# Optimization experiments

Hardware: AMD Instinct MI355X
Metric: run time of the kernel (lower is better)

## Reference

```python
import jax, jax.numpy as jnp
import numpy as np
import math

D_MODEL = 1024
NUM_HEADS = 16
HEAD_DIM = D_MODEL // NUM_HEADS
B, T = 2, 2048


def _linear_params(key, d_in, d_out):
    kw, kb = jax.random.split(key)
    s = 1.0 / math.sqrt(d_in)
    W = jax.random.uniform(kw, (d_in, d_out), jnp.float32, -s, s)
    b = jax.random.uniform(kb, (d_out,), jnp.float32, -s, s)
    return W, b


def setup_inputs() -> dict:
    key = jax.random.key(0)
    ks = jax.random.split(key, 10)
    x_real = jax.random.normal(ks[0], (B, T, D_MODEL), jnp.float32)
    x_imag = jax.random.normal(ks[1], (B, T, D_MODEL), jnp.float32)
    Wqr, bqr = _linear_params(ks[2], D_MODEL, D_MODEL)
    Wqi, bqi = _linear_params(ks[3], D_MODEL, D_MODEL)
    Wkr, bkr = _linear_params(ks[4], D_MODEL, D_MODEL)
    Wki, bki = _linear_params(ks[5], D_MODEL, D_MODEL)
    Wvr, bvr = _linear_params(ks[6], D_MODEL, D_MODEL)
    Wvi, bvi = _linear_params(ks[7], D_MODEL, D_MODEL)
    Wor, bor = _linear_params(ks[8], D_MODEL, D_MODEL)
    Woi, boi = _linear_params(ks[9], D_MODEL, D_MODEL)
    return dict(x_real=x_real, x_imag=x_imag,
                Wqr=Wqr, bqr=bqr, Wqi=Wqi, bqi=bqi,
                Wkr=Wkr, bkr=bkr, Wki=Wki, bki=bki,
                Wvr=Wvr, bvr=bvr, Wvi=Wvi, bvi=bvi,
                Wor=Wor, bor=bor, Woi=Woi, boi=boi)


def _heads(x):
    # (B,T,C) -> (B,H,T,Dh)
    b, t, _ = x.shape
    return x.reshape(b, t, NUM_HEADS, HEAD_DIM).transpose(0, 2, 1, 3)


def reference(x_real, x_imag,
              Wqr, bqr, Wqi, bqi, Wkr, bkr, Wki, bki,
              Wvr, bvr, Wvi, bvi, Wor, bor, Woi, boi):
    b, t, c = x_real.shape
    # NOTE: first two qr/qi assignments in the torch forward are dead code;
    # effective math is below.
    qr = _heads(x_real @ Wqr + bqr)
    qi = _heads(x_imag @ Wqi + bqi)
    kr = _heads(x_real @ Wkr + bkr)
    ki = _heads(x_imag @ Wki + bki)
    vr = _heads(x_real @ Wvr + bvr)
    vi = _heads(x_imag @ Wvi + bvi)
    # Re(Q K^H) score: Qr*Kr + Qi*Ki, scaled
    score = (jnp.einsum('bhtd,bhsd->bhts', qr, kr)
             + jnp.einsum('bhtd,bhsd->bhts', qi, ki)) / math.sqrt(HEAD_DIM)
    causal = jnp.triu(jnp.ones((t, t), dtype=bool), k=1)  # True above diagonal
    score = jnp.where(causal[None, None], -jnp.inf, score)
    attn = jax.nn.softmax(score, axis=-1)
    out_r = jnp.einsum('bhts,bhsd->bhtd', attn, vr).transpose(0, 2, 1, 3).reshape(b, t, c)
    out_i = jnp.einsum('bhts,bhsd->bhtd', attn, vi).transpose(0, 2, 1, 3).reshape(b, t, c)
    final_r = out_r @ Wor + bor
    final_i = out_i @ Woi + boi
    return (final_r, final_i)
```

## Files before the change

kernel.cpp:

```cpp
#include <hip/hip_runtime.h>
#include <hip/hip_bf16.h>


typedef __attribute__((ext_vector_type(8))) __bf16 bf16x8;
typedef __attribute__((ext_vector_type(4))) float f32x4;
typedef unsigned short u16;

#define L2E 1.44269504088896340736f

__device__ __forceinline__ void gl2lds16(const void* g, void* l) {
  __builtin_amdgcn_global_load_lds(
      (const __attribute__((address_space(1))) unsigned int*)g,
      (__attribute__((address_space(3))) unsigned int*)l, 16, 0, 0);
}

__device__ __forceinline__ u16 f2bf(float f) {
  union { float f; unsigned u; } v;
  v.f = f;
  unsigned r = v.u + 0x7FFFu + ((v.u >> 16) & 1u);
  return (u16)(r >> 16);
}

__global__ void cvt_bf16_2(const float* __restrict__ a, const float* __restrict__ bsrc,
                           u16* __restrict__ oa, u16* __restrict__ ob, int n) {
  const float* in = blockIdx.y ? bsrc : a;
  u16* out = blockIdx.y ? ob : oa;
  int stride = gridDim.x * blockDim.x * 4;
  for (int i = (blockIdx.x * blockDim.x + threadIdx.x) * 4; i < n; i += stride) {
    float4 v = *(const float4*)(in + i);
    ushort4 o;
    o.x = f2bf(v.x); o.y = f2bf(v.y); o.z = f2bf(v.z); o.w = f2bf(v.w);
    *(ushort4*)(out + i) = o;
  }
}

struct WPtrs { const float* w[8]; };

__global__ void cvt_w_t(WPtrs ptrs, u16* __restrict__ out) {
  __shared__ float tile[32][33];
  const float* W = ptrs.w[blockIdx.z];
  u16* o = out + ((size_t)blockIdx.z << 20);
  int tx = threadIdx.x & 31, ty = threadIdx.x >> 5;
  int bx = blockIdx.x * 32, by = blockIdx.y * 32;
#pragma unroll
  for (int k = 0; k < 4; k++) {
    int r = by + ty + k * 8;
    tile[ty + k * 8][tx] = W[(size_t)r * 1024 + bx + tx];
  }
  __syncthreads();
#pragma unroll
  for (int k = 0; k < 4; k++) {
    int n = bx + ty + k * 8;
    o[(size_t)n * 1024 + by + tx] = f2bf(tile[tx][ty + k * 8]);
  }
}

struct GemmArgs {
  const u16* A[6];
  const u16* Wt[6];
  const float* bias[6];
  void* dst[6];
  int off[6];
  float scale[6];
};

template <int MODE>
__global__ __launch_bounds__(256, 2) void gemm_bf16(GemmArgs args) {
  extern __shared__ u16 dynpad[];
  const int z = blockIdx.z;
  const u16* __restrict__ A = args.A[z];
  const u16* __restrict__ Bt = args.Wt[z];
  const float* __restrict__ bias = args.bias[z];
  const int brow = blockIdx.x * 128;
  const int bcol = blockIdx.y * 128;

  __shared__ u16 lA[2][128 * 32];
  __shared__ u16 lB[2][128 * 32];

  const int tid = threadIdx.x;
  const int w = tid >> 6, lane = tid & 63;
  const int wrow = (w >> 1) * 64, wcol = (w & 1) * 64;

  if (args.off[z] == -12345) ((volatile u16*)dynpad)[0] = 0;

  f32x4 acc[4][4] = {};

  auto stage = [&](int buf, int t) {
    int k0 = t * 32;
#pragma unroll
    for (int s = 0; s < 2; s++) {
      int q = w * 2 + s;
      int lr = q * 16 + (lane >> 2);
      int csrc = (lane & 3) ^ ((lr >> 1) & 3);
      gl2lds16(A + (size_t)(brow + lr) * 1024 + k0 + csrc * 8, &lA[buf][q * 512]);
    }
#pragma unroll
    for (int s = 0; s < 2; s++) {
      int q = w * 2 + s;
      int lr = q * 16 + (lane >> 2);
      int csrc = (lane & 3) ^ ((lr >> 1) & 3);
      gl2lds16(Bt + (size_t)(bcol + lr) * 1024 + k0 + csrc * 8, &lB[buf][q * 512]);
    }
  };

  stage(0, 0);
  __syncthreads();

  int buf = 0;
  for (int t = 0; t < 32; t++) {
    if (t + 1 < 32) stage(buf ^ 1, t + 1);
    bf16x8 a[4], b[4];
#pragma unroll
    for (int i = 0; i < 4; i++) {
      int row = wrow + i * 16 + (lane & 15);
      int cs = (lane >> 4) ^ ((row >> 1) & 3);
      a[i] = *(const bf16x8*)&lA[buf][row * 32 + cs * 8];
      int col = wcol + i * 16 + (lane & 15);
      int cs2 = (lane >> 4) ^ ((col >> 1) & 3);
      b[i] = *(const bf16x8*)&lB[buf][col * 32 + cs2 * 8];
    }
#pragma unroll
    for (int i = 0; i < 4; i++)
#pragma unroll
      for (int j = 0; j < 4; j++)
        acc[i][j] = __builtin_amdgcn_mfma_f32_16x16x32_bf16(a[i], b[j], acc[i][j], 0, 0, 0);
    __syncthreads();
    buf ^= 1;
  }

  const int off = args.off[z];
  const float scl = args.scale[z];
#pragma unroll
  for (int i = 0; i < 4; i++)
#pragma unroll
    for (int j = 0; j < 4; j++)
#pragma unroll
      for (int r = 0; r < 4; r++) {
        int grow = brow + wrow + i * 16 + (lane >> 4) * 4 + r;
        int gcol = bcol + wcol + j * 16 + (lane & 15);
        float v = (acc[i][j][r] + bias[gcol]) * scl;
        if (MODE == 0) {
          ((float*)args.dst[z])[(size_t)grow * 1024 + gcol] = v;
        } else {
          int bb = grow >> 11, tt = grow & 2047;
          int h = gcol >> 6, dh = gcol & 63;
          ((u16*)args.dst[z])[(((size_t)(bb * 16 + h) * 2048 + tt) << 7) + off + dh] = f2bf(v);
        }
      }
}

__global__ void transpose_v(const u16* __restrict__ Vc, u16* __restrict__ Vt) {
  __shared__ u16 tile[64 * 64];
  const int bh = blockIdx.z, t0 = blockIdx.x * 64, d0 = blockIdx.y * 64;
  const int tid = threadIdx.x;
  const int tl = tid >> 3, c = tid & 7;
#pragma unroll
  for (int hh = 0; hh < 2; hh++) {
    int t = tl + hh * 32;
    int sc = c ^ (t & 7) ^ ((t >> 3) & 7);
    *(bf16x8*)&tile[t * 64 + sc * 8] =
        *(const bf16x8*)&Vc[((size_t)bh * 2048 + t0 + t) * 128 + d0 + c * 8];
  }
  __syncthreads();
#pragma unroll
  for (int hh = 0; hh < 2; hh++) {
    int d = tl + hh * 32;
    bf16x8 v;
#pragma unroll
    for (int j = 0; j < 8; j++) {
      int t = c * 8 + j;
      int sc = (d >> 3) ^ (t & 7) ^ ((t >> 3) & 7);
      v[j] = ((const __bf16*)tile)[t * 64 + sc * 8 + (d & 7)];
    }
    *(bf16x8*)&Vt[((size_t)bh * 128 + d0 + d) * 2048 + t0 + c * 8] = v;
  }
}

__global__ __launch_bounds__(256, 2) void attn_kernel(
    const u16* __restrict__ Q, const u16* __restrict__ K, const u16* __restrict__ Vt,
    u16* __restrict__ Or, u16* __restrict__ Oi) {
  const int bh = blockIdx.x;
  const int ii = (int)gridDim.y - 1 - (int)blockIdx.y;
  const int tid = threadIdx.x, w = tid >> 6, lane = tid & 63;
  const int ql = lane & 15, hi = lane >> 4;
  const int b = bh >> 4, h = bh & 15;

  __shared__ u16 lK[2][64 * 128];
  __shared__ u16 lV[2][128 * 64];
  __shared__ u16 lP[4][16 * 64];

  const int qrow0 = ii * 64 + w * 16;
  const int q = qrow0 + ql;

  bf16x8 qf[4];
#pragma unroll
  for (int kk = 0; kk < 4; kk++)
    qf[kk] = *(const bf16x8*)(Q + ((size_t)bh * 2048 + q) * 128 + kk * 32 + hi * 8);

  f32x4 o[8] = {};
  float l = 0.f;

  const int ntiles = ii + 1;

  auto stageKV = [&](int buf, int jt) {
#pragma unroll
    for (int s = 0; s < 4; s++) {
      int seg = w * 4 + s;
      int srow = seg * 4 + (lane >> 4);
      int csrc = (lane & 15) ^ (srow & 15);
      gl2lds16(K + ((size_t)bh * 2048 + jt * 64 + srow) * 128 + csrc * 8, &lK[buf][seg * 512]);
    }
#pragma unroll
    for (int s = 0; s < 4; s++) {
      int seg = w * 4 + s;
      int dv = seg * 8 + (lane >> 3);
      int csrc = (lane & 7) ^ (dv & 7);
      gl2lds16(Vt + ((size_t)bh * 128 + dv) * 2048 + jt * 64 + csrc * 8, &lV[buf][seg * 512]);
    }
  };

  stageKV(0, 0);
  __syncthreads();

  int buf = 0;
  for (int jt = 0; jt < ntiles; jt++) {
    if (jt + 1 < ntiles) stageKV(buf ^ 1, jt + 1);

    f32x4 s[4] = {};
    __builtin_amdgcn_s_setprio(1);
#pragma unroll
    for (int kk = 0; kk < 4; kk++) {
#pragma unroll
      for (int j = 0; j < 4; j++) {
        int sl = j * 16 + ql;
        int cs = (kk * 4 + hi) ^ (sl & 15);
        bf16x8 kf = *(const bf16x8*)&lK[buf][sl * 128 + cs * 8];
        s[j] = __builtin_amdgcn_mfma_f32_16x16x32_bf16(kf, qf[kk], s[j], 0, 0, 0);
      }
    }
    __builtin_amdgcn_s_setprio(0);

    if (jt == ii) {
#pragma unroll
      for (int j = 0; j < 4; j++)
#pragma unroll
        for (int r = 0; r < 4; r++) {
          int kg = jt * 64 + j * 16 + hi * 4 + r;
          if (kg > q) s[j][r] = -__builtin_inff();
        }
    }

    uint2 pk[4];
#pragma unroll
    for (int j = 0; j < 4; j++) {
      float p0 = exp2f(__builtin_fmaf(s[j][0], L2E, -16.f * L2E));
      float p1 = exp2f(__builtin_fmaf(s[j][1], L2E, -16.f * L2E));
      float p2 = exp2f(__builtin_fmaf(s[j][2], L2E, -16.f * L2E));
      float p3 = exp2f(__builtin_fmaf(s[j][3], L2E, -16.f * L2E));
      l += (p0 + p1) + (p2 + p3);
      union { __bf16 hh[4]; uint2 u; } cv;
      cv.hh[0] = (__bf16)p0; cv.hh[1] = (__bf16)p1;
      cv.hh[2] = (__bf16)p2; cv.hh[3] = (__bf16)p3;
      pk[j] = cv.u;
    }

#pragma unroll
    for (int j = 0; j < 4; j++) {
      int byte_off = ql * 128 + ((j * 32 + hi * 8) ^ ((ql & 7) << 4));
      *(uint2*)((char*)&lP[w][0] + byte_off) = pk[j];
    }
    asm volatile("s_waitcnt lgkmcnt(0)" ::: "memory");
    __builtin_amdgcn_sched_barrier(0);

    __builtin_amdgcn_s_setprio(1);
#pragma unroll
    for (int kks = 0; kks < 2; kks++) {
      int pb = ql * 128 + ((kks * 64 + hi * 16) ^ ((ql & 7) << 4));
      bf16x8 pf = *(const bf16x8*)((char*)&lP[w][0] + pb);
#pragma unroll
      for (int jv = 0; jv < 8; jv++) {
        int dv = jv * 16 + ql;
        int cs = (kks * 4 + hi) ^ (dv & 7);
        bf16x8 vf = *(const bf16x8*)&lV[buf][dv * 64 + cs * 8];
        o[jv] = __builtin_amdgcn_mfma_f32_16x16x32_bf16(vf, pf, o[jv], 0, 0, 0);
      }
    }
    __builtin_amdgcn_s_setprio(0);

    __syncthreads();
    buf ^= 1;
  }

  l += __shfl_xor(l, 16);
  l += __shfl_xor(l, 32);
  float linv = 1.f / l;
  const size_t obase = ((size_t)b * 2048 + q) * 1024 + h * 64;
#pragma unroll
  for (int jv = 0; jv < 8; jv++) {
    ushort4 st;
    union { __bf16 hh[4]; ushort4 u; } cv;
    cv.hh[0] = (__bf16)(o[jv][0] * linv);
    cv.hh[1] = (__bf16)(o[jv][1] * linv);
    cv.hh[2] = (__bf16)(o[jv][2] * linv);
    cv.hh[3] = (__bf16)(o[jv][3] * linv);
    st = cv.u;
    u16* dst = (jv < 4) ? Or : Oi;
    *(ushort4*)(dst + obase + (jv & 3) * 16 + hi * 4) = st;
  }
}

extern "C" void kernel_launch(void* const* d_in, const int* in_sizes, int n_in,
                              void* d_out, int out_size, void* d_ws, size_t ws_size,
                              hipStream_t stream) {
  (void)in_sizes; (void)n_in; (void)out_size; (void)ws_size;

  const float* x_real = (const float*)d_in[0];
  const float* x_imag = (const float*)d_in[1];

  char* ws = (char*)d_ws;
  size_t off = 0;
  auto alloc = [&](size_t bytes) {
    void* p = ws + off;
    off += (bytes + 255) & ~(size_t)255;
    return p;
  };
  const size_t MK = 4096ull * 1024;
  u16* xr16 = (u16*)alloc(MK * 2);
  u16* xi16 = (u16*)alloc(MK * 2);
  u16* Wt   = (u16*)alloc(8ull * 1024 * 1024 * 2);
  u16* Qc   = (u16*)alloc(32ull * 2048 * 128 * 2);
  u16* Kc   = (u16*)alloc(32ull * 2048 * 128 * 2);
  u16* Vc   = (u16*)alloc(32ull * 2048 * 128 * 2);
  u16* Vt   = (u16*)alloc(32ull * 2048 * 128 * 2);
  u16* Or   = Vc;
  u16* Oi   = Vc + MK;

  cvt_bf16_2<<<dim3(1024, 2), 256, 0, stream>>>(x_real, x_imag, xr16, xi16, (int)MK);

  WPtrs wp;
  wp.w[0] = (const float*)d_in[2];
  wp.w[1] = (const float*)d_in[4];
  wp.w[2] = (const float*)d_in[6];
  wp.w[3] = (const float*)d_in[8];
  wp.w[4] = (const float*)d_in[10];
  wp.w[5] = (const float*)d_in[12];
  wp.w[6] = (const float*)d_in[14];
  wp.w[7] = (const float*)d_in[16];
  cvt_w_t<<<dim3(32, 32, 8), 256, 0, stream>>>(wp, Wt);

  GemmArgs pa{};
  const u16* xs[2] = {xr16, xi16};
  for (int z = 0; z < 6; z++) {
    pa.A[z] = xs[z & 1];
    pa.Wt[z] = Wt + (size_t)z * 1048576;
    pa.off[z] = (z & 1) * 64;
    pa.scale[z] = (z < 2) ? 0.125f : 1.0f;
  }
  pa.bias[0] = (const float*)d_in[3];
  pa.bias[1] = (const float*)d_in[5];
  pa.bias[2] = (const float*)d_in[7];
  pa.bias[3] = (const float*)d_in[9];
  pa.bias[4] = (const float*)d_in[11];
  pa.bias[5] = (const float*)d_in[13];
  pa.dst[0] = Qc; pa.dst[1] = Qc;
  pa.dst[2] = Kc; pa.dst[3] = Kc;
  pa.dst[4] = Vc; pa.dst[5] = Vc;
  gemm_bf16<1><<<dim3(32, 8, 6), 256, 16384, stream>>>(pa);

  transpose_v<<<dim3(32, 2, 32), 256, 0, stream>>>(Vc, Vt);

  attn_kernel<<<dim3(32, 32), 256, 0, stream>>>(Qc, Kc, Vt, Or, Oi);

  GemmArgs fa{};
  fa.A[0] = Or; fa.A[1] = Oi;
  fa.Wt[0] = Wt + 6ull * 1048576;
  fa.Wt[1] = Wt + 7ull * 1048576;
  fa.bias[0] = (const float*)d_in[15];
  fa.bias[1] = (const float*)d_in[17];
  fa.dst[0] = (float*)d_out;
  fa.dst[1] = (float*)d_out + MK;
  fa.off[0] = 0; fa.off[1] = 0;
  fa.scale[0] = 1.0f; fa.scale[1] = 1.0f;
  gemm_bf16<0><<<dim3(32, 8, 2), 256, 16384, stream>>>(fa);
}
```

Baseline: 182.1 us.

## Rewrite projection GEMMs with 512-thread 256x128 tiles and triple-buffered K=64 pipeline

Replaces the 128x128 double-buffered GEMM with a 512-thread (8-wave) kernel computing 256x128 tiles, using K-steps of 64 and a 3-slot LDS ring that prefetches two steps ahead with explicit vmcnt waits and raw barriers. Loads of A and B are interleaved between the two MFMA halves, and s_setprio raises wave priority during MFMA bursts. The goal is to hide global-to-LDS latency and halve barrier count per K. LDS use grows to about 144KB per block, which likely limits occupancy to one block per CU, and the grid shrinks so there are fewer blocks for the final 2-matrix GEMM.

Measured after the change: 190.9 us. +4.8%, slower.

```diff
diff --git a/kernel.cpp b/kernel.cpp
--- a/kernel.cpp
+++ b/kernel.cpp
@@ -65,67 +65,103 @@
 };
 
 template <int MODE>
-__global__ __launch_bounds__(256, 2) void gemm_bf16(GemmArgs args) {
-  extern __shared__ u16 dynpad[];
+__global__ __launch_bounds__(512, 2) void gemm8p(GemmArgs args) {
   const int z = blockIdx.z;
   const u16* __restrict__ A = args.A[z];
   const u16* __restrict__ Bt = args.Wt[z];
   const float* __restrict__ bias = args.bias[z];
-  const int brow = blockIdx.x * 128;
+  const int brow = blockIdx.x * 256;
   const int bcol = blockIdx.y * 128;
 
-  __shared__ u16 lA[2][128 * 32];
-  __shared__ u16 lB[2][128 * 32];
+  __shared__ u16 lA[3][256 * 64];
+  __shared__ u16 lB[3][128 * 64];
 
   const int tid = threadIdx.x;
   const int w = tid >> 6, lane = tid & 63;
-  const int wrow = (w >> 1) * 64, wcol = (w & 1) * 64;
-
-  if (args.off[z] == -12345) ((volatile u16*)dynpad)[0] = 0;
+  const int ql = lane & 15, hi = lane >> 4;
+  const int wr = w >> 1, wc = w & 1;
 
   f32x4 acc[4][4] = {};
 
-  auto stage = [&](int buf, int t) {
-    int k0 = t * 32;
-#pragma unroll
-    for (int s = 0; s < 2; s++) {
-      int q = w * 2 + s;
-      int lr = q * 16 + (lane >> 2);
-      int csrc = (lane & 3) ^ ((lr >> 1) & 3);
-      gl2lds16(A + (size_t)(brow + lr) * 1024 + k0 + csrc * 8, &lA[buf][q * 512]);
-    }
-#pragma unroll
-    for (int s = 0; s < 2; s++) {
-      int q = w * 2 + s;
-      int lr = q * 16 + (lane >> 2);
-      int csrc = (lane & 3) ^ ((lr >> 1) & 3);
-      gl2lds16(Bt + (size_t)(bcol + lr) * 1024 + k0 + csrc * 8, &lB[buf][q * 512]);
+  auto stageA = [&](int kt, int slot) {
+    int k0 = kt * 64;
+#pragma unroll
+    for (int g = 0; g < 4; g++) {
+      int row = g * 64 + w * 8 + (lane >> 3);
+      int csrc = (lane & 7) ^ (row & 7);
+      gl2lds16(A + (size_t)(brow + row) * 1024 + k0 + csrc * 8,
+               &lA[slot][(g * 64 + w * 8) * 64]);
     }
   };
-
-  stage(0, 0);
-  __syncthreads();
-
-  int buf = 0;
-  for (int t = 0; t < 32; t++) {
-    if (t + 1 < 32) stage(buf ^ 1, t + 1);
+  auto stageB = [&](int kt, int slot) {
+    int k0 = kt * 64;
+#pragma unroll
+    for (int g = 0; g < 2; g++) {
+      int row = g * 64 + w * 8 + (lane >> 3);
+      int csrc = (lane & 7) ^ (row & 7);
+      gl2lds16(Bt + (size_t)(bcol + row) * 1024 + k0 + csrc * 8,
+               &lB[slot][(g * 64 + w * 8) * 64]);
+    }
+  };
+
+  stageA(0, 0); stageB(0, 0);
+  stageA(1, 1); stageB(1, 1);
+  asm volatile("s_waitcnt vmcnt(6)" ::: "memory");
+  __builtin_amdgcn_s_barrier();
+
+  for (int kt = 0; kt < 16; kt++) {
+    const int slot = kt % 3;
+    const int pre = (kt + 2) % 3;
+    const bool more = (kt + 2) < 16;
+
+    if (more) stageA(kt + 2, pre);
+
     bf16x8 a[4], b[4];
 #pragma unroll
     for (int i = 0; i < 4; i++) {
-      int row = wrow + i * 16 + (lane & 15);
-      int cs = (lane >> 4) ^ ((row >> 1) & 3);
-      a[i] = *(const bf16x8*)&lA[buf][row * 32 + cs * 8];
-      int col = wcol + i * 16 + (lane & 15);
-      int cs2 = (lane >> 4) ^ ((col >> 1) & 3);
-      b[i] = *(const bf16x8*)&lB[buf][col * 32 + cs2 * 8];
-    }
+      int row = wr * 64 + i * 16 + ql;
+      int c = hi ^ (row & 7);
+      a[i] = *(const bf16x8*)&lA[slot][row * 64 + c * 8];
+    }
+#pragma unroll
+    for (int j = 0; j < 4; j++) {
+      int row = wc * 64 + j * 16 + ql;
+      int c = hi ^ (row & 7);
+      b[j] = *(const bf16x8*)&lB[slot][row * 64 + c * 8];
+    }
+    __builtin_amdgcn_s_setprio(1);
 #pragma unroll
     for (int i = 0; i < 4; i++)
 #pragma unroll
       for (int j = 0; j < 4; j++)
         acc[i][j] = __builtin_amdgcn_mfma_f32_16x16x32_bf16(a[i], b[j], acc[i][j], 0, 0, 0);
-    __syncthreads();
-    buf ^= 1;
+    __builtin_amdgcn_s_setprio(0);
+
+    if (more) stageB(kt + 2, pre);
+
+#pragma unroll
+    for (int i = 0; i < 4; i++) {
+      int row = wr * 64 + i * 16 + ql;
+      int c = (4 + hi) ^ (row & 7);
+      a[i] = *(const bf16x8*)&lA[slot][row * 64 + c * 8];
+    }
+#pragma unroll
+    for (int j = 0; j < 4; j++) {
+      int row = wc * 64 + j * 16 + ql;
+      int c = (4 + hi) ^ (row & 7);
+      b[j] = *(const bf16x8*)&lB[slot][row * 64 + c * 8];
+    }
+    __builtin_amdgcn_s_setprio(1);
+#pragma unroll
+    for (int i = 0; i < 4; i++)
+#pragma unroll
+      for (int j = 0; j < 4; j++)
+        acc[i][j] = __builtin_amdgcn_mfma_f32_16x16x32_bf16(a[i], b[j], acc[i][j], 0, 0, 0);
+    __builtin_amdgcn_s_setprio(0);
+
+    if (kt <= 13)      asm volatile("s_waitcnt vmcnt(6)" ::: "memory");
+    else if (kt == 14) asm volatile("s_waitcnt vmcnt(0)" ::: "memory");
+    if (kt < 15) __builtin_amdgcn_s_barrier();
   }
 
   const int off = args.off[z];
@@ -133,12 +169,13 @@
 #pragma unroll
   for (int i = 0; i < 4; i++)
 #pragma unroll
-    for (int j = 0; j < 4; j++)
+    for (int j = 0; j < 4; j++) {
+      int gcol = bcol + wc * 64 + j * 16 + ql;
+      float bv = bias[gcol];
 #pragma unroll
       for (int r = 0; r < 4; r++) {
-        int grow = brow + wrow + i * 16 + (lane >> 4) * 4 + r;
-        int gcol = bcol + wcol + j * 16 + (lane & 15);
-        float v = (acc[i][j][r] + bias[gcol]) * scl;
+        int grow = brow + wr * 64 + i * 16 + hi * 4 + r;
+        float v = (acc[i][j][r] + bv) * scl;
         if (MODE == 0) {
           ((float*)args.dst[z])[(size_t)grow * 1024 + gcol] = v;
         } else {
@@ -147,6 +184,7 @@
           ((u16*)args.dst[z])[(((size_t)(bb * 16 + h) * 2048 + tt) << 7) + off + dh] = f2bf(v);
         }
       }
+    }
 }
 
 __global__ void transpose_v(const u16* __restrict__ Vc, u16* __restrict__ Vt) {
@@ -365,7 +403,7 @@
   pa.dst[0] = Qc; pa.dst[1] = Qc;
   pa.dst[2] = Kc; pa.dst[3] = Kc;
   pa.dst[4] = Vc; pa.dst[5] = Vc;
-  gemm_bf16<1><<<dim3(32, 8, 6), 256, 16384, stream>>>(pa);
+  gemm8p<1><<<dim3(16, 8, 6), 512, 0, stream>>>(pa);
 
   transpose_v<<<dim3(32, 2, 32), 256, 0, stream>>>(Vc, Vt);
 
@@ -381,5 +419,5 @@
   fa.dst[1] = (float*)d_out + MK;
   fa.off[0] = 0; fa.off[1] = 0;
   fa.scale[0] = 1.0f; fa.scale[1] = 1.0f;
-  gemm_bf16<0><<<dim3(32, 8, 2), 256, 16384, stream>>>(fa);
-}
+  gemm8p<0><<<dim3(16, 8, 2), 512, 0, stream>>>(fa);
+}
```
